# Kernel tuning notes

Measured on AMD Instinct MI355X. Metric: run time of the kernel, lower is better.

Reference implementation:

```python
import jax, jax.numpy as jnp
import numpy as np

D_MODEL = 384
D_STATE = 64
D_CONV = 3
EXPAND = 2
HEADDIM = 64
NGROUPS = 1
CHUNK = 256
D_INNER = EXPAND * D_MODEL            # 768
NHEADS = D_INNER // HEADDIM           # 12
CONV_DIM = D_INNER + 2 * NGROUPS * D_STATE   # 896
D_IN_PROJ = 2 * D_INNER + 2 * NGROUPS * D_STATE + NHEADS  # 1676
EPS = 1e-5


def setup_inputs() -> dict:
    key = jax.random.key(0)
    ks = jax.random.split(key, 8)
    B, H, W = 16, 32, 32
    u = jax.random.normal(ks[0], (B, D_MODEL, H, W), jnp.float32)
    in_proj_w = jax.random.normal(ks[1], (D_IN_PROJ, D_MODEL), jnp.float32) / np.sqrt(D_MODEL)
    conv_w = jax.random.normal(ks[2], (CONV_DIM, 1, D_CONV, D_CONV), jnp.float32) / np.sqrt(D_CONV * D_CONV)
    conv_b = jax.random.normal(ks[3], (CONV_DIM,), jnp.float32) * 0.01
    # dt_bias init as in Mamba2.__init__
    dt = jnp.exp(jax.random.uniform(ks[4], (NHEADS,)) * (np.log(0.1) - np.log(0.001)) + np.log(0.001))
    dt = jnp.clip(dt, 1e-4, None)
    dt_bias = dt + jnp.log(-jnp.expm1(-dt))
    A_log = jnp.log(jax.random.uniform(ks[5], (NHEADS,), minval=1.0, maxval=16.0))
    D = jnp.ones((NHEADS,), jnp.float32)
    norm_w = jnp.ones((D_INNER,), jnp.float32)
    norm_b = jnp.zeros((D_INNER,), jnp.float32)
    out_proj_w = jax.random.normal(ks[6], (D_MODEL, D_INNER), jnp.float32) / np.sqrt(D_INNER)
    return {"u": u, "in_proj_w": in_proj_w, "conv_w": conv_w, "conv_b": conv_b,
            "dt_bias": dt_bias, "A_log": A_log, "D": D, "norm_w": norm_w,
            "norm_b": norm_b, "out_proj_w": out_proj_w}


def _chunk_scan(x, dt, A, Bm, Cm):
    """SSD chunked scan. x:(b,l,h,p) dt:(b,l,h) A:(h,) Bm,Cm:(b,l,g,n) -> (b,l,h,p)"""
    b, l, h, p = x.shape
    nc = l // CHUNK
    xc = x.reshape(b, nc, CHUNK, h, p)
    dtc = dt.reshape(b, nc, CHUNK, h)
    hpg = h // NGROUPS
    Bh = jnp.repeat(Bm.reshape(b, nc, CHUNK, NGROUPS, D_STATE), hpg, axis=3)  # (b,c,cs,h,n)
    Ch = jnp.repeat(Cm.reshape(b, nc, CHUNK, NGROUPS, D_STATE), hpg, axis=3)
    dA = dtc * A                                  # (b,c,cs,h)
    dA_cs = jnp.cumsum(dA, axis=2)                # cumulative log-decay within chunk
    # ---- intra-chunk (masked, attention-like) ----
    Lmat = jnp.exp(dA_cs[:, :, :, None, :] - dA_cs[:, :, None, :, :])  # (b,c,i,j,h)
    causal = jnp.tril(jnp.ones((CHUNK, CHUNK), bool))
    att = jnp.einsum('bcihn,bcjhn->bcijh', Ch, Bh) * Lmat * dtc[:, :, None, :, :]
    att = jnp.where(causal[None, None, :, :, None], att, 0.0)
    y_intra = jnp.einsum('bcijh,bcjhp->bcihp', att, xc)
    # ---- per-chunk end states ----
    decay_to_end = jnp.exp(dA_cs[:, :, -1:, :] - dA_cs)                 # (b,c,cs,h)
    states = jnp.einsum('bcjhn,bcjh,bcjhp->bchpn', Bh, decay_to_end * dtc, xc)
    chunk_decay = jnp.exp(dA_cs[:, :, -1, :])                           # (b,c,h)
    # ---- inter-chunk recurrence over the (few) chunks ----
    def step(carry, inp):
        st, dec = inp
        new = carry * dec[:, :, None, None] + st
        return new, carry  # emit state *before* this chunk
    init = jnp.zeros((b, h, p, D_STATE), x.dtype)
    _, prevs = jax.lax.scan(step, init, (jnp.moveaxis(states, 1, 0), jnp.moveaxis(chunk_decay, 1, 0)))
    prev_states = jnp.moveaxis(prevs, 0, 1)                             # (b,c,h,p,n)
    y_inter = jnp.einsum('bcihn,bcih,bchpn->bcihp', Ch, jnp.exp(dA_cs), prev_states)
    return (y_intra + y_inter).reshape(b, l, h, p)


def reference(u, in_proj_w, conv_w, conv_b, dt_bias, A_log, D, norm_w, norm_b, out_proj_w):
    B, C, H, W = u.shape
    L = H * W
    useq = u.reshape(B, C, L).transpose(0, 2, 1)                        # (B,L,C)
    zxbcdt = useq @ in_proj_w.T                                         # (B,L,D_IN_PROJ)
    z = zxbcdt[..., :D_INNER]
    xBC = zxbcdt[..., D_INNER:D_INNER + CONV_DIM]
    dt = jax.nn.softplus(zxbcdt[..., D_INNER + CONV_DIM:] + dt_bias)    # (B,L,NHEADS)
    # depthwise 3x3 conv over (H,W)
    xBC = xBC.reshape(B, H, W, CONV_DIM)
    kern = jnp.transpose(conv_w, (2, 3, 1, 0))                          # HWIO, groups=CONV_DIM
    xBC = jax.lax.conv_general_dilated(xBC, kern, (1, 1), 'SAME',
                                       dimension_numbers=('NHWC', 'HWIO', 'NHWC'),
                                       feature_group_count=CONV_DIM) + conv_b
    xBC = jax.nn.silu(xBC).reshape(B, L, CONV_DIM)
    x = xBC[..., :D_INNER].reshape(B, L, NHEADS, HEADDIM)
    Bm = xBC[..., D_INNER:D_INNER + NGROUPS * D_STATE].reshape(B, L, NGROUPS, D_STATE)
    Cm = xBC[..., D_INNER + NGROUPS * D_STATE:].reshape(B, L, NGROUPS, D_STATE)
    A = -jnp.exp(A_log)
    y = _chunk_scan(x, dt, A, Bm, Cm) + D[None, None, :, None] * x      # D skip per head
    y = y.reshape(B, L, D_INNER)
    # LayerNorm then gate by z (no activation on z, matching source)
    mu = jnp.mean(y, axis=-1, keepdims=True)
    var = jnp.var(y, axis=-1, keepdims=True)
    y = (y - mu) / jnp.sqrt(var + EPS) * norm_w + norm_b
    y = y * z
    out = y @ out_proj_w.T                                              # (B,L,C)
    return out.reshape(B, H, W, C).transpose(0, 3, 1, 2)
```

## Files before the change

### kernel.cpp

```cpp
#include <hip/hip_runtime.h>
#include <hip/hip_bf16.h>

#define B_    16
#define L_    1024
#define DM    384
#define DIP   1676
#define NIP   1664
#define DI    768
#define CONVD 896
#define NH    12
#define HD    64
#define DS    64
#define NCH   4
#define CH    256
#define EPS_  1e-5f

typedef unsigned short u16;
typedef unsigned int   u32;
typedef __attribute__((ext_vector_type(8))) _Float16 f16x8;
typedef __attribute__((ext_vector_type(4))) float f32x4;

union U4 { uint4 v; u16 s[8]; };

#define SWZ(row, slot) (((row) << 7) + ((((slot) ^ ((row) & 7)) & 7) << 4))

__device__ __forceinline__ u16 f2h(float v) { return __builtin_bit_cast(u16, (_Float16)v); }
__device__ __forceinline__ float h2f(u16 h) { return (float)__builtin_bit_cast(_Float16, h); }
__device__ __forceinline__ void hsplit(float v, u16& h, u16& l) {
  _Float16 hh = (_Float16)v;
  _Float16 ll = (_Float16)(v - (float)hh);
  h = __builtin_bit_cast(u16, hh);
  l = __builtin_bit_cast(u16, ll);
}

__global__ __launch_bounds__(256) void k_cvtA(const float* __restrict__ u,
                                              u16* __restrict__ Ah)
{
  __shared__ float Ls[32][129];
  const int t  = threadIdx.x;
  const int l0 = blockIdx.x * 128;
  const int k0 = blockIdx.y * 32;
  const int b  = blockIdx.z;
#pragma unroll
  for (int r = 0; r < 4; ++r) {
    int idx = r * 256 + t;
    int kk = idx >> 5, q = idx & 31;
    float4 v = *(const float4*)&u[((size_t)(b * DM + k0 + kk)) * L_ + l0 + q * 4];
    Ls[kk][q * 4 + 0] = v.x; Ls[kk][q * 4 + 1] = v.y;
    Ls[kk][q * 4 + 2] = v.z; Ls[kk][q * 4 + 3] = v.w;
  }
  __syncthreads();
#pragma unroll
  for (int it = 0; it < 2; ++it) {
    int task = it * 256 + t;
    int l = task >> 2, kq = (task & 3) * 8;
    u32 hw[4];
#pragma unroll
    for (int j = 0; j < 4; ++j) {
      u16 h0 = f2h(Ls[kq + 2 * j + 0][l]);
      u16 h1 = f2h(Ls[kq + 2 * j + 1][l]);
      hw[j] = (u32)h0 | ((u32)h1 << 16);
    }
    size_t off = ((size_t)(b * L_ + l0 + l)) * DM + k0 + kq;
    *(uint4*)&Ah[off] = make_uint4(hw[0], hw[1], hw[2], hw[3]);
  }
}

__global__ __launch_bounds__(256) void k_cvtWh(const float* __restrict__ W,
                                               u16* __restrict__ Wh, int total4)
{
  int i = blockIdx.x * 256 + threadIdx.x;
  if (i >= total4) return;
  int e = i * 4;
  float4 v = *(const float4*)&W[e];
  u16 h[4] = {f2h(v.x), f2h(v.y), f2h(v.z), f2h(v.w)};
  *(uint2*)&Wh[e] = make_uint2((u32)h[0] | ((u32)h[1] << 16), (u32)h[2] | ((u32)h[3] << 16));
}

__global__ __launch_bounds__(256) void k_dtp(
    const float* __restrict__ u, const float* __restrict__ ipw,
    const float* __restrict__ dtb, const float* __restrict__ A_log,
    float* __restrict__ dt, float* __restrict__ dAcs, float* __restrict__ cdecay)
{
  __shared__ float wdt[DM];
  __shared__ float ws4[4];
  const int bc = blockIdx.x;
  const int h  = blockIdx.y;
  const int b  = bc >> 2, l0 = (bc & 3) * 256;
  const int t  = threadIdx.x;
  const int lane = t & 63, w = t >> 6;
  for (int i = t; i < DM; i += 256) wdt[i] = ipw[(size_t)(NIP + h) * DM + i];
  __syncthreads();
  const float* ub = u + (size_t)b * DM * L_ + l0 + t;
  float acc = 0.f;
#pragma unroll 8
  for (int k = 0; k < DM; ++k)
    acc = fmaf(ub[(size_t)k * L_], wdt[k], acc);
  const size_t row = (size_t)bc * 256 + t;
  float logit = acc + dtb[h];
  float dtv = (logit > 20.f) ? logit : log1pf(expf(logit));
  dt[row * NH + h] = dtv;
  float xv = dtv * (-expf(A_log[h]));
#pragma unroll
  for (int off = 1; off < 64; off <<= 1) {
    float y = __shfl_up(xv, off, 64);
    if (lane >= off) xv += y;
  }
  if (lane == 63) ws4[w] = xv;
  __syncthreads();
  float add = 0.f;
#pragma unroll
  for (int i = 0; i < 4; ++i) if (i < w) add += ws4[i];
  xv += add;
  dAcs[row * NH + h] = xv;
  if (t == 255) cdecay[bc * NH + h] = expf(xv);
}

#define STAGE2(bufbase, k0) do {                                                                \
  _Pragma("unroll")                                                                             \
  for (int i_ = 0; i_ < 2; ++i_) {                                                              \
    int S_ = i_ * 256 + t;                                                                      \
    int m_ = S_ >> 2;                                                                           \
    int g_ = (S_ ^ (m_ >> 1)) & 3;                                                              \
    size_t goff_ = (size_t)m_ * DM + (k0) + g_ * 8;                                             \
    __builtin_amdgcn_global_load_lds((const __attribute__((address_space(1))) u32*)(g0 + goff_),\
        (__attribute__((address_space(3))) u32*)(lds + (bufbase) + S_ * 8), 16, 0, 0);          \
    __builtin_amdgcn_global_load_lds((const __attribute__((address_space(1))) u32*)(g2 + goff_),\
        (__attribute__((address_space(3))) u32*)(lds + (bufbase) + 4096 + S_ * 8), 16, 0, 0);   \
  }                                                                                             \
} while (0)

__global__ __launch_bounds__(256) void k_gemm1(
    const u16* __restrict__ Ah,
    const u16* __restrict__ Wh,
    u16* __restrict__ z, u16* __restrict__ xBC)
{
  __shared__ u16 lds[16384];
  const int t = threadIdx.x;
  const int lane = t & 63, wid = t >> 6;
  const int wr = wid >> 1, wc = wid & 1;
  const int gg = lane >> 4, mlo = lane & 15;
  const int m0 = blockIdx.x * 128, n0 = blockIdx.y * 128;
  f32x4 acc[4][4];
#pragma unroll
  for (int i = 0; i < 4; ++i)
#pragma unroll
    for (int j = 0; j < 4; ++j) acc[i][j] = (f32x4){0.f, 0.f, 0.f, 0.f};
  const u16* g0 = Ah + (size_t)m0 * DM;
  const u16* g2 = Wh + (size_t)n0 * DM;
  STAGE2(0, 0);
  __syncthreads();
  int cur = 0;
  for (int kt = 0; kt < DM / 32; ++kt) {
    if (kt + 1 < DM / 32) STAGE2((cur ^ 1) * 8192, (kt + 1) * 32);
    const char* ldsb = (const char*)lds + cur * 16384;
    f16x8 fa[4], fb[4];
#pragma unroll
    for (int mf = 0; mf < 4; ++mf) {
      int m = wr * 64 + mf * 16 + mlo;
      int off = m * 64 + (((gg ^ (m >> 1)) & 3) << 4);
      fa[mf]  = *(const f16x8*)(ldsb + off);
    }
#pragma unroll
    for (int nf = 0; nf < 4; ++nf) {
      int n = wc * 64 + nf * 16 + mlo;
      int off = n * 64 + (((gg ^ (n >> 1)) & 3) << 4);
      fb[nf]  = *(const f16x8*)(ldsb + 8192 + off);
    }
#pragma unroll
    for (int mf = 0; mf < 4; ++mf)
#pragma unroll
      for (int nf = 0; nf < 4; ++nf)
        acc[mf][nf] = __builtin_amdgcn_mfma_f32_16x16x32_f16(fa[mf], fb[nf], acc[mf][nf], 0, 0, 0);
    __syncthreads();
    cur ^= 1;
  }
  const int rb = m0 + wr * 64 + (lane >> 4) * 4;
  const int cb = n0 + wc * 64 + mlo;
#pragma unroll
  for (int mf = 0; mf < 4; ++mf)
#pragma unroll
    for (int nf = 0; nf < 4; ++nf) {
      int col = cb + nf * 16;
#pragma unroll
      for (int r = 0; r < 4; ++r) {
        int row = rb + mf * 16 + r;
        float v = acc[mf][nf][r];
        if (col < DI) z[(size_t)row * DI + col] = f2h(v);
        else xBC[(size_t)row * CONVD + (col - DI)] = f2h(v);
      }
    }
}

#define STAGE3B(bufbase, k0) do {                                                               \
  _Pragma("unroll")                                                                             \
  for (int i_ = 0; i_ < 2; ++i_) {                                                              \
    int S_ = i_ * 256 + t;                                                                      \
    int m_ = S_ >> 2;                                                                           \
    int g_ = (S_ ^ (m_ >> 1)) & 3;                                                              \
    size_t goff_ = (size_t)m_ * DI + (k0) + g_ * 8;                                             \
    __builtin_amdgcn_global_load_lds((const __attribute__((address_space(1))) u32*)(g0 + goff_),\
        (__attribute__((address_space(3))) u32*)(lds + (bufbase) + S_ * 8), 16, 0, 0);          \
    __builtin_amdgcn_global_load_lds((const __attribute__((address_space(1))) u32*)(g1 + goff_),\
        (__attribute__((address_space(3))) u32*)(lds + (bufbase) + 4096 + S_ * 8), 16, 0, 0);   \
    __builtin_amdgcn_global_load_lds((const __attribute__((address_space(1))) u32*)(g2 + goff_),\
        (__attribute__((address_space(3))) u32*)(lds + (bufbase) + 8192 + S_ * 8), 16, 0, 0);   \
  }                                                                                             \
} while (0)

__global__ __launch_bounds__(256) void k_gemm2(
    const u16* __restrict__ Ah, const u16* __restrict__ Al,
    const u16* __restrict__ Bh,
    float* __restrict__ out)
{
  __shared__ u16 lds[24576];
  const int t = threadIdx.x;
  const int lane = t & 63, wid = t >> 6;
  const int wr = wid >> 1, wc = wid & 1;
  const int gg = lane >> 4, mlo = lane & 15;
  const int m0 = blockIdx.x * 128, n0 = blockIdx.y * 128;
  f32x4 acc[4][4];
#pragma unroll
  for (int i = 0; i < 4; ++i)
#pragma unroll
    for (int j = 0; j < 4; ++j) acc[i][j] = (f32x4){0.f, 0.f, 0.f, 0.f};
  const u16* g0 = Ah + (size_t)m0 * DI;
  const u16* g1 = Al + (size_t)m0 * DI;
  const u16* g2 = Bh + (size_t)n0 * DI;
  STAGE3B(0, 0);
  __syncthreads();
  int cur = 0;
  for (int kt = 0; kt < DI / 32; ++kt) {
    if (kt + 1 < DI / 32) STAGE3B((cur ^ 1) * 12288, (kt + 1) * 32);
    const char* ldsb = (const char*)lds + cur * 24576;
    f16x8 fa[4], fal[4], fb[4];
#pragma unroll
    for (int mf = 0; mf < 4; ++mf) {
      int m = wr * 64 + mf * 16 + mlo;
      int off = m * 64 + (((gg ^ (m >> 1)) & 3) << 4);
      fa[mf]  = *(const f16x8*)(ldsb + off);
      fal[mf] = *(const f16x8*)(ldsb + 8192 + off);
    }
#pragma unroll
    for (int nf = 0; nf < 4; ++nf) {
      int n = wc * 64 + nf * 16 + mlo;
      int off = n * 64 + (((gg ^ (n >> 1)) & 3) << 4);
      fb[nf]  = *(const f16x8*)(ldsb + 16384 + off);
    }
#pragma unroll
    for (int mf = 0; mf < 4; ++mf)
#pragma unroll
      for (int nf = 0; nf < 4; ++nf) {
        acc[mf][nf] = __builtin_amdgcn_mfma_f32_16x16x32_f16(fa[mf],  fb[nf], acc[mf][nf], 0, 0, 0);
        acc[mf][nf] = __builtin_amdgcn_mfma_f32_16x16x32_f16(fal[mf], fb[nf], acc[mf][nf], 0, 0, 0);
      }
    __syncthreads();
    cur ^= 1;
  }
  const int rb = m0 + wr * 64 + (lane >> 4) * 4;
  const int cb = n0 + wc * 64 + mlo;
#pragma unroll
  for (int mf = 0; mf < 4; ++mf)
#pragma unroll
    for (int nf = 0; nf < 4; ++nf) {
      int col = cb + nf * 16;
#pragma unroll
      for (int r = 0; r < 4; ++r) {
        int row = rb + mf * 16 + r;
        int b = row >> 10, l = row & 1023;
        out[((size_t)(b * DM + col)) * L_ + l] = acc[mf][nf][r];
      }
    }
}

#define CC 16
__global__ __launch_bounds__(256) void k_conv(
    const u16* __restrict__ xBC, const float* __restrict__ cw,
    const float* __restrict__ cb,
    u16* __restrict__ XTh,
    u16* __restrict__ Bh,
    u16* __restrict__ Chh)
{
  __shared__ float Ls[18][32][CC];
  const int t  = threadIdx.x;
  const int c0 = blockIdx.x * CC;
  const int h0 = blockIdx.y * 16;
  const int b  = blockIdx.z;
#pragma unroll
  for (int k = 0; k < 9; ++k) {
    int f = k * 256 + t;
    int fc4 = f & 3, fw = (f >> 2) & 31, fr = f >> 7;
    int h = h0 + fr - 1;
    U4 v; v.v = make_uint4(0, 0, 0, 0);
    if (h >= 0 && h < 32) {
      uint2 p = *(const uint2*)&xBC[((size_t)(b * 1024 + h * 32 + fw)) * CONVD + c0 + fc4 * 4];
      v.v.x = p.x; v.v.y = p.y;
    }
    Ls[fr][fw][fc4 * 4 + 0] = h2f(v.s[0]);
    Ls[fr][fw][fc4 * 4 + 1] = h2f(v.s[1]);
    Ls[fr][fw][fc4 * 4 + 2] = h2f(v.s[2]);
    Ls[fr][fw][fc4 * 4 + 3] = h2f(v.s[3]);
  }
  const int c4 = t & 3;
  const int w  = (t >> 2) & 31;
  const int hb = t >> 7;
  float wt[4][9];
  float bias[4];
#pragma unroll
  for (int j = 0; j < 4; ++j) {
    int c = c0 + c4 * 4 + j;
    bias[j] = cb[c];
#pragma unroll
    for (int kb = 0; kb < 9; ++kb) wt[j][kb] = cw[c * 9 + kb];
  }
  __syncthreads();
  const bool isx = (c0 < DI);
  u16 xh16[8][4];
#pragma unroll
  for (int k = 0; k < 8; ++k) {
    int h = hb * 8 + k;
    float acc[4] = {bias[0], bias[1], bias[2], bias[3]};
#pragma unroll
    for (int dh = 0; dh < 3; ++dh) {
#pragma unroll
      for (int dw = -1; dw <= 1; ++dw) {
        int ww = w + dw;
        if (ww < 0 || ww > 31) continue;
        const float* p = &Ls[h + dh][ww][c4 * 4];
        int kb = dh * 3 + (dw + 1);
#pragma unroll
        for (int j = 0; j < 4; ++j) acc[j] = fmaf(p[j], wt[j][kb], acc[j]);
      }
    }
    float s4[4];
#pragma unroll
    for (int j = 0; j < 4; ++j) { float v = acc[j]; s4[j] = v / (1.f + expf(-v)); }
    if (isx) {
#pragma unroll
      for (int j = 0; j < 4; ++j) xh16[k][j] = f2h(s4[j]);
    } else {
      size_t row = (size_t)b * 1024 + (h0 + h) * 32 + w;
      u16 hv[4] = {f2h(s4[0]), f2h(s4[1]), f2h(s4[2]), f2h(s4[3])};
      uint2 hp = make_uint2((u32)hv[0] | ((u32)hv[1] << 16), (u32)hv[2] | ((u32)hv[3] << 16));
      int c = c0 + c4 * 4;
      if (c < DI + DS) *(uint2*)&Bh[row * DS + (c - DI)] = hp;
      else             *(uint2*)&Chh[row * DS + (c - DI - DS)] = hp;
    }
  }
  if (isx) {
    __syncthreads();
    u16* Ls2 = (u16*)Ls;
#pragma unroll
    for (int k = 0; k < 8; ++k) {
      int pos = (hb * 8 + k) * 32 + w;
#pragma unroll
      for (int j = 0; j < 4; ++j)
        Ls2[(c4 * 4 + j) * 512 + pos] = xh16[k][j];
    }
    __syncthreads();
    const int hh = c0 >> 6;
    const int pb = c0 & 63;
#pragma unroll
    for (int i = 0; i < 4; ++i) {
      int cid = i * 256 + t;
      int pl = cid >> 6, rem = cid & 63;
      int jbl = rem >> 3, slot = rem & 7;
      int labs = h0 * 32 + jbl * 64;
      size_t tile = ((size_t)(b * 4 + (labs >> 8)) * NH + hh) * 4 + ((labs >> 6) & 3);
      *(uint4*)((char*)XTh + tile * 8192 + SWZ(pb + pl, slot)) =
          *(const uint4*)&Ls2[pl * 512 + jbl * 64 + slot * 8];
    }
  }
}

#define STAGE_XT(tileByte) do {                                                                   \
  _Pragma("unroll")                                                                               \
  for (int i_ = 0; i_ < 2; ++i_) {                                                                \
    int S_ = i_ * 256 + t;                                                                        \
    __builtin_amdgcn_global_load_lds(                                                             \
        (const __attribute__((address_space(1))) u32*)((const char*)XTh + (tileByte) + S_ * 16),  \
        (__attribute__((address_space(3))) u32*)((char*)Xh_t + S_ * 16), 16, 0, 0);               \
  }                                                                                               \
} while (0)

__global__ __launch_bounds__(256) void k_states(
    const u16* __restrict__ XTh,
    const u16* __restrict__ Bh,
    const float* __restrict__ dt, const float* __restrict__ dAcs,
    float* __restrict__ states)
{
  __shared__ u16 bpackB[64 * 65];
  __shared__ u16 BTh_t[4096];
  __shared__ u16 Xh_t[4096];
  __shared__ float wall[256];
  const int bc = blockIdx.x;
  const int hh = blockIdx.y;
  const int t  = threadIdx.x;
  const int lane = t & 63, w = t >> 6;
  const int mlo = lane & 15, gg = lane >> 4;
  const int r = t >> 2, q = (t & 3) * 16;
  const size_t base = (size_t)bc * 256;
  const float last = dAcs[(base + 255) * NH + hh];
  wall[t] = __expf(last - dAcs[(base + t) * NH + hh]) * dt[(base + t) * NH + hh];
  f32x4 acc[4];
#pragma unroll
  for (int i = 0; i < 4; ++i) acc[i] = (f32x4){0.f, 0.f, 0.f, 0.f};
  for (int jt = 0; jt < 4; ++jt) {
    const int j0 = jt * 64;
    __syncthreads();
    STAGE_XT(((size_t)(bc * NH + hh) * 4 + jt) * 8192);
    {
      const u16* bhp = &Bh[(size_t)(base + j0 + r) * DS + q];
      U4 H0, H1;
      H0.v = *(const uint4*)bhp; H1.v = *(const uint4*)(bhp + 8);
#pragma unroll
      for (int k = 0; k < 8; ++k) {
        bpackB[r * 65 + q + k]     = H0.s[k];
        bpackB[r * 65 + q + 8 + k] = H1.s[k];
      }
    }
    __syncthreads();
#pragma unroll
    for (int c = 0; c < 2; ++c) {
      U4 BH;
#pragma unroll
      for (int jj = 0; jj < 8; ++jj) {
        int j = q + c * 8 + jj;
        BH.s[jj] = f2h(h2f(bpackB[j * 65 + r]) * wall[j0 + j]);
      }
      *(uint4*)((char*)BTh_t + SWZ(r, (q >> 3) + c)) = BH.v;
    }
    __syncthreads();
#pragma unroll
    for (int s = 0; s < 2; ++s) {
      f16x8 fah = *(const f16x8*)((const char*)Xh_t + SWZ(w * 16 + mlo, s * 4 + gg));
#pragma unroll
      for (int nf = 0; nf < 4; ++nf) {
        f16x8 fbh = *(const f16x8*)((const char*)BTh_t + SWZ(nf * 16 + mlo, s * 4 + gg));
        acc[nf] = __builtin_amdgcn_mfma_f32_16x16x32_f16(fah, fbh, acc[nf], 0, 0, 0);
      }
    }
  }
  const size_t sb = ((size_t)(bc * NH + hh)) << 12;
#pragma unroll
  for (int nf = 0; nf < 4; ++nf)
#pragma unroll
    for (int reg = 0; reg < 4; ++reg) {
      int p = w * 16 + (lane >> 4) * 4 + reg;
      int n = nf * 16 + mlo;
      states[sb + (size_t)p * 64 + n] = acc[nf][reg];
    }
}

__global__ __launch_bounds__(256) void k_scanc(
    const float* __restrict__ states, const float* __restrict__ cdecay,
    float* __restrict__ prev)
{
  int tid = blockIdx.x * 256 + threadIdx.x;
  int pn  = tid & 4095;
  int rem = tid >> 12;
  int hh  = rem % NH;
  int b   = rem / NH;
  float carry = 0.f;
#pragma unroll
  for (int c = 0; c < 4; ++c) {
    size_t idx = ((size_t)((b * 4 + c) * NH + hh) << 12) + pn;
    prev[idx] = carry;
    carry = carry * cdecay[(b * 4 + c) * NH + hh] + states[idx];
  }
}

__global__ __launch_bounds__(256) void k_y(
    const u16* __restrict__ XTh,
    const u16* __restrict__ Chg, const u16* __restrict__ Bhg,
    const float* __restrict__ dtp, const float* __restrict__ dAcs,
    const float* __restrict__ prev, const float* __restrict__ Dp,
    u16* __restrict__ y)
{
  __shared__ u16 Pb_t[4096];
  __shared__ u16 Xh_t[4096];
  __shared__ u16 att_t[4096];
  __shared__ float dAc_s[256], dt_s[256], ei_s[128];
  const int bc = blockIdx.x;
  const int hh = blockIdx.y;
  const int z  = blockIdx.z;
  const int it0 = z * 2;
  const int t  = threadIdx.x;
  const int lane = t & 63, w = t >> 6;
  const int mlo = lane & 15, gg = lane >> 4;
  const int r = t >> 2, q = (t & 3) * 16;
  const int slot0 = q >> 3;
  const size_t base = (size_t)bc * 256;
  {
    float da = dAcs[(base + t) * NH + hh];
    dAc_s[t] = da;
    dt_s[t]  = dtp[(base + t) * NH + hh];
    if (t < 128) ei_s[t] = __expf(dAcs[(base + z * 128 + t) * NH + hh]);
  }
  {
    const float* pp = &prev[(((size_t)(bc * NH + hh)) << 12) + (size_t)r * 64 + q];
    U4 H0, H1;
#pragma unroll
    for (int k = 0; k < 16; ++k) {
      u16 h = f2h(pp[k]);
      if (k < 8) H0.s[k] = h; else H1.s[k - 8] = h;
    }
    *(uint4*)((char*)Pb_t + SWZ(r, slot0))     = H0.v;
    *(uint4*)((char*)Pb_t + SWZ(r, slot0 + 1)) = H1.v;
  }
  __syncthreads();
  f16x8 fc[2][2];
#pragma unroll
  for (int iti = 0; iti < 2; ++iti)
#pragma unroll
    for (int s = 0; s < 2; ++s)
      fc[iti][s] = *(const f16x8*)&Chg[(size_t)(base + (it0 + iti) * 64 + w * 16 + mlo) * DS +
                                       (s * 4 + gg) * 8];
  f32x4 accy[2][4];
#pragma unroll
  for (int i = 0; i < 2; ++i)
#pragma unroll
    for (int j = 0; j < 4; ++j) accy[i][j] = (f32x4){0.f, 0.f, 0.f, 0.f};
#pragma unroll
  for (int s = 0; s < 2; ++s)
#pragma unroll
    for (int pf = 0; pf < 4; ++pf) {
      f16x8 fph = *(const f16x8*)((const char*)Pb_t + SWZ(pf * 16 + mlo, s * 4 + gg));
#pragma unroll
      for (int iti = 0; iti < 2; ++iti)
        accy[iti][pf] = __builtin_amdgcn_mfma_f32_16x16x32_f16(fc[iti][s], fph, accy[iti][pf], 0, 0, 0);
    }
  const int ilb = w * 16 + (lane >> 4) * 4;
#pragma unroll
  for (int iti = 0; iti < 2; ++iti)
#pragma unroll
    for (int pf = 0; pf < 4; ++pf)
#pragma unroll
      for (int reg = 0; reg < 4; ++reg)
        accy[iti][pf][reg] *= ei_s[iti * 64 + ilb + reg];

  u32 xdv[2][8];
  for (int jt = 0; jt <= it0 + 1; ++jt) {
    __syncthreads();
    STAGE_XT(((size_t)(bc * NH + hh) * 4 + jt) * 8192);
    {
      const u16* bh = &Bhg[(size_t)(base + jt * 64 + r) * DS + q];
      U4 V0, V1;
      V0.v = *(const uint4*)bh; V1.v = *(const uint4*)(bh + 8);
      float wj = dt_s[jt * 64 + r];
#pragma unroll
      for (int k = 0; k < 8; ++k) {
        V0.s[k] = f2h(h2f(V0.s[k]) * wj);
        V1.s[k] = f2h(h2f(V1.s[k]) * wj);
      }
      *(uint4*)((char*)Pb_t + SWZ(r, slot0))     = V0.v;
      *(uint4*)((char*)Pb_t + SWZ(r, slot0 + 1)) = V1.v;
    }
    __syncthreads();
#pragma unroll
    for (int iti = 0; iti < 2; ++iti) {
      if (jt == it0 + iti) {
#pragma unroll
        for (int pf = 0; pf < 4; ++pf)
#pragma unroll
          for (int rp = 0; rp < 2; ++rp) {
            int j0l = ilb + rp * 2;
            u16 a = *(const u16*)((const char*)Xh_t + SWZ(pf * 16 + mlo, j0l >> 3) + (j0l & 7) * 2);
            u16 b2 = *(const u16*)((const char*)Xh_t + SWZ(pf * 16 + mlo, (j0l + 1) >> 3) + ((j0l + 1) & 7) * 2);
            xdv[iti][pf * 2 + rp] = (u32)a | ((u32)b2 << 16);
          }
      }
    }
#pragma unroll
    for (int iti = 0; iti < 2; ++iti) {
      const int ita = it0 + iti;
      if (jt > ita) continue;
      f32x4 g[4];
#pragma unroll
      for (int i = 0; i < 4; ++i) g[i] = (f32x4){0.f, 0.f, 0.f, 0.f};
#pragma unroll
      for (int s = 0; s < 2; ++s)
#pragma unroll
        for (int jf = 0; jf < 4; ++jf) {
          f16x8 fbh = *(const f16x8*)((const char*)Pb_t + SWZ(jf * 16 + mlo, s * 4 + gg));
          g[jf] = __builtin_amdgcn_mfma_f32_16x16x32_f16(fc[iti][s], fbh, g[jf], 0, 0, 0);
        }
#pragma unroll
      for (int jf = 0; jf < 4; ++jf)
#pragma unroll
        for (int reg = 0; reg < 4; ++reg) {
          int il = ita * 64 + ilb + reg;
          int jl = jt * 64 + jf * 16 + mlo;
          float av = (jl <= il) ? g[jf][reg] * __expf(dAc_s[il] - dAc_s[jl]) : 0.f;
          *(u16*)((char*)att_t + SWZ(il & 63, (jl & 63) >> 3) + (jl & 7) * 2) = f2h(av);
        }
#pragma unroll
      for (int s = 0; s < 2; ++s) {
        f16x8 fa = *(const f16x8*)((const char*)att_t + SWZ(w * 16 + mlo, s * 4 + gg));
#pragma unroll
        for (int pf = 0; pf < 4; ++pf) {
          f16x8 fxh = *(const f16x8*)((const char*)Xh_t + SWZ(pf * 16 + mlo, s * 4 + gg));
          accy[iti][pf] = __builtin_amdgcn_mfma_f32_16x16x32_f16(fa, fxh, accy[iti][pf], 0, 0, 0);
        }
      }
    }
  }
  const float Dh = Dp[hh];
#pragma unroll
  for (int iti = 0; iti < 2; ++iti)
#pragma unroll
    for (int pf = 0; pf < 4; ++pf)
#pragma unroll
      for (int reg = 0; reg < 4; ++reg) {
        size_t row = base + (it0 + iti) * 64 + ilb + reg;
        int col = hh * HD + pf * 16 + mlo;
        u32 pk = xdv[iti][pf * 2 + (reg >> 1)];
        u16 xv = (reg & 1) ? (u16)(pk >> 16) : (u16)pk;
        y[row * DI + col] = f2h(accy[iti][pf][reg] + Dh * h2f(xv));
      }
}

__global__ __launch_bounds__(256) void k_norm(
    const u16* __restrict__ z, const float* __restrict__ nw,
    const float* __restrict__ nb, const u16* __restrict__ y,
    u16* __restrict__ yh, u16* __restrict__ yl)
{
  __shared__ float rs[4], rq[4];
  const size_t row = blockIdx.x;
  const int t = threadIdx.x;
  float v[3];
  float s = 0.f, sq = 0.f;
#pragma unroll
  for (int r = 0; r < 3; ++r) {
    v[r] = h2f(y[row * DI + r * 256 + t]);
    s += v[r];
    sq = fmaf(v[r], v[r], sq);
  }
#pragma unroll
  for (int off = 32; off > 0; off >>= 1) {
    s  += __shfl_down(s, off, 64);
    sq += __shfl_down(sq, off, 64);
  }
  const int wid = t >> 6, lane = t & 63;
  if (lane == 0) { rs[wid] = s; rq[wid] = sq; }
  __syncthreads();
  if (t == 0) {
    rs[0] = rs[0] + rs[1] + rs[2] + rs[3];
    rq[0] = rq[0] + rq[1] + rq[2] + rq[3];
  }
  __syncthreads();
  const float mu   = rs[0] * (1.f / DI);
  const float var  = rq[0] * (1.f / DI) - mu * mu;
  const float rstd = 1.f / sqrtf(var + EPS_);
#pragma unroll
  for (int r = 0; r < 3; ++r) {
    int d = r * 256 + t;
    float o = (v[r] - mu) * rstd * nw[d] + nb[d];
    float p = o * h2f(z[row * DI + d]);
    u16 h, l;
    hsplit(p, h, l);
    yh[row * DI + d] = h;
    yl[row * DI + d] = l;
  }
}

extern "C" void kernel_launch(void* const* d_in, const int* in_sizes, int n_in,
                              void* d_out, int out_size, void* d_ws, size_t ws_size,
                              hipStream_t stream)
{
  const float* u    = (const float*)d_in[0];
  const float* ipw  = (const float*)d_in[1];
  const float* cw   = (const float*)d_in[2];
  const float* cb   = (const float*)d_in[3];
  const float* dtb  = (const float*)d_in[4];
  const float* Alog = (const float*)d_in[5];
  const float* Dp   = (const float*)d_in[6];
  const float* nw   = (const float*)d_in[7];
  const float* nb   = (const float*)d_in[8];
  const float* opw  = (const float*)d_in[9];
  float* out = (float*)d_out;

  float* ws = (float*)d_ws;
  size_t off = 0;
  u16*   z16     = (u16*)(ws + off); off += (size_t)B_ * L_ * DI / 2;
  u16*   xBC16   = (u16*)(ws + off); off += (size_t)B_ * L_ * CONVD / 2;
  float* dt_buf  = ws + off; off += (size_t)B_ * L_ * NH;
  float* x_buf   = ws + off; off += (size_t)B_ * L_ * DI;
  u16*   y16     = (u16*)(ws + off); off += (size_t)B_ * L_ * DI / 2;
  u16*   Bh_buf  = (u16*)(ws + off); off += (size_t)B_ * L_ * DS / 2;
  u16*   Ch_buf  = (u16*)(ws + off); off += (size_t)B_ * L_ * DS / 2;
  float* dAcs    = ws + off; off += (size_t)B_ * L_ * NH;
  float* cdec    = ws + off; off += (size_t)B_ * NCH * NH;
  float* st_buf  = ws + off; off += (size_t)B_ * NCH * NH * HD * DS;
  float* pv_buf  = ws + off; off += (size_t)B_ * NCH * NH * HD * DS;
  u16*   Woh     = (u16*)(ws + off); off += (size_t)DM * DI / 2;
  u16*   XTh_buf = (u16*)(ws + off); off += (size_t)B_ * NCH * NH * 4 * 4096 / 2;

  u16* Ah = (u16*)x_buf;
  u16* Whip = Ah + (size_t)B_ * L_ * DM;
  u16* yh = (u16*)x_buf;
  u16* yl = yh + (size_t)B_ * L_ * DI;

  hipLaunchKernelGGL(k_cvtA, dim3(8, 12, 16), dim3(256), 0, stream, u, Ah);
  hipLaunchKernelGGL(k_cvtWh, dim3((NIP * DM / 4 + 255) / 256), dim3(256), 0, stream,
                     ipw, Whip, NIP * DM / 4);
  hipLaunchKernelGGL(k_cvtWh, dim3((DM * DI / 4 + 255) / 256), dim3(256), 0, stream,
                     opw, Woh, DM * DI / 4);
  hipLaunchKernelGGL(k_dtp, dim3(64, 12), dim3(256), 0, stream,
                     u, ipw, dtb, Alog, dt_buf, dAcs, cdec);
  hipLaunchKernelGGL(k_gemm1, dim3(128, 13), dim3(256), 0, stream,
                     Ah, Whip, z16, xBC16);
  hipLaunchKernelGGL(k_conv, dim3(56, 2, 16), dim3(256), 0, stream,
                     xBC16, cw, cb, XTh_buf, Bh_buf, Ch_buf);
  hipLaunchKernelGGL(k_states, dim3(64, 12), dim3(256), 0, stream,
                     XTh_buf, Bh_buf, dt_buf, dAcs, st_buf);
  hipLaunchKernelGGL(k_scanc, dim3(3072), dim3(256), 0, stream, st_buf, cdec, pv_buf);
  hipLaunchKernelGGL(k_y, dim3(64, 12, 2), dim3(256), 0, stream,
                     XTh_buf, Ch_buf, Bh_buf, dt_buf, dAcs, pv_buf, Dp, y16);
  hipLaunchKernelGGL(k_norm, dim3(16384), dim3(256), 0, stream, z16, nw, nb, y16, yh, yl);
  hipLaunchKernelGGL(k_gemm2, dim3(128, 3), dim3(256), 0, stream, yh, yl, Woh, out);
}
```

Measured before the change: 205.1 us.

## Deepen gemm1 LDS pipeline to four buffers and merge k_y z-split blocks

In k_gemm1, the double-buffered K loop becomes a 4-slot ring buffer with two tiles prefetched ahead. Each step waits with a partial vmcnt and one raw barrier instead of two __syncthreads, so more load latency can be hidden at the cost of doubling LDS per block. In k_y, the two z-blocks per (chunk, head) are merged into one block that handles all four 64-row tiles. This removes the duplicated staging of X and B tiles (z=1 previously restaged tiles 0-1) but halves the grid to 768 blocks and doubles the accumulator registers.

```diff
diff --git a/kernel.cpp b/kernel.cpp
--- a/kernel.cpp
+++ b/kernel.cpp
@@ -135,7 +135,7 @@
     const u16* __restrict__ Wh,
     u16* __restrict__ z, u16* __restrict__ xBC)
 {
-  __shared__ u16 lds[16384];
+  __shared__ u16 lds[32768];
   const int t = threadIdx.x;
   const int lane = t & 63, wid = t >> 6;
   const int wr = wid >> 1, wc = wid & 1;
@@ -148,12 +148,15 @@
     for (int j = 0; j < 4; ++j) acc[i][j] = (f32x4){0.f, 0.f, 0.f, 0.f};
   const u16* g0 = Ah + (size_t)m0 * DM;
   const u16* g2 = Wh + (size_t)n0 * DM;
-  STAGE2(0, 0);
-  __syncthreads();
-  int cur = 0;
-  for (int kt = 0; kt < DM / 32; ++kt) {
-    if (kt + 1 < DM / 32) STAGE2((cur ^ 1) * 8192, (kt + 1) * 32);
-    const char* ldsb = (const char*)lds + cur * 16384;
+  const int NT = DM / 32;
+  STAGE2(0 * 8192, 0 * 32);
+  STAGE2(1 * 8192, 1 * 32);
+  for (int kt = 0; kt < NT; ++kt) {
+    int ks = kt + 2; if (ks > NT - 1) ks = NT - 1;
+    STAGE2(((kt + 2) & 3) * 8192, ks * 32);
+    asm volatile("s_waitcnt vmcnt(8)" ::: "memory");
+    __builtin_amdgcn_s_barrier();
+    const char* ldsb = (const char*)lds + (kt & 3) * 16384;
     f16x8 fa[4], fb[4];
 #pragma unroll
     for (int mf = 0; mf < 4; ++mf) {
@@ -172,8 +175,6 @@
 #pragma unroll
       for (int nf = 0; nf < 4; ++nf)
         acc[mf][nf] = __builtin_amdgcn_mfma_f32_16x16x32_f16(fa[mf], fb[nf], acc[mf][nf], 0, 0, 0);
-    __syncthreads();
-    cur ^= 1;
   }
   const int rb = m0 + wr * 64 + (lane >> 4) * 4;
   const int cb = n0 + wc * 64 + mlo;
@@ -480,11 +481,9 @@
   __shared__ u16 Pb_t[4096];
   __shared__ u16 Xh_t[4096];
   __shared__ u16 att_t[4096];
-  __shared__ float dAc_s[256], dt_s[256], ei_s[128];
+  __shared__ float dAc_s[256], dt_s[256], ei_s[256];
   const int bc = blockIdx.x;
   const int hh = blockIdx.y;
-  const int z  = blockIdx.z;
-  const int it0 = z * 2;
   const int t  = threadIdx.x;
   const int lane = t & 63, w = t >> 6;
   const int mlo = lane & 15, gg = lane >> 4;
@@ -495,7 +494,7 @@
     float da = dAcs[(base + t) * NH + hh];
     dAc_s[t] = da;
     dt_s[t]  = dtp[(base + t) * NH + hh];
-    if (t < 128) ei_s[t] = __expf(dAcs[(base + z * 128 + t) * NH + hh]);
+    ei_s[t]  = __expf(da);
   }
   {
     const float* pp = &prev[(((size_t)(bc * NH + hh)) << 12) + (size_t)r * 64 + q];
@@ -509,16 +508,16 @@
     *(uint4*)((char*)Pb_t + SWZ(r, slot0 + 1)) = H1.v;
   }
   __syncthreads();
-  f16x8 fc[2][2];
-#pragma unroll
-  for (int iti = 0; iti < 2; ++iti)
+  f16x8 fc[4][2];
+#pragma unroll
+  for (int iti = 0; iti < 4; ++iti)
 #pragma unroll
     for (int s = 0; s < 2; ++s)
-      fc[iti][s] = *(const f16x8*)&Chg[(size_t)(base + (it0 + iti) * 64 + w * 16 + mlo) * DS +
+      fc[iti][s] = *(const f16x8*)&Chg[(size_t)(base + iti * 64 + w * 16 + mlo) * DS +
                                        (s * 4 + gg) * 8];
-  f32x4 accy[2][4];
-#pragma unroll
-  for (int i = 0; i < 2; ++i)
+  f32x4 accy[4][4];
+#pragma unroll
+  for (int i = 0; i < 4; ++i)
 #pragma unroll
     for (int j = 0; j < 4; ++j) accy[i][j] = (f32x4){0.f, 0.f, 0.f, 0.f};
 #pragma unroll
@@ -527,20 +526,20 @@
     for (int pf = 0; pf < 4; ++pf) {
       f16x8 fph = *(const f16x8*)((const char*)Pb_t + SWZ(pf * 16 + mlo, s * 4 + gg));
 #pragma unroll
-      for (int iti = 0; iti < 2; ++iti)
+      for (int iti = 0; iti < 4; ++iti)
         accy[iti][pf] = __builtin_amdgcn_mfma_f32_16x16x32_f16(fc[iti][s], fph, accy[iti][pf], 0, 0, 0);
     }
   const int ilb = w * 16 + (lane >> 4) * 4;
 #pragma unroll
-  for (int iti = 0; iti < 2; ++iti)
+  for (int iti = 0; iti < 4; ++iti)
 #pragma unroll
     for (int pf = 0; pf < 4; ++pf)
 #pragma unroll
       for (int reg = 0; reg < 4; ++reg)
         accy[iti][pf][reg] *= ei_s[iti * 64 + ilb + reg];
 
-  u32 xdv[2][8];
-  for (int jt = 0; jt <= it0 + 1; ++jt) {
+  u32 xdv[4][8];
+  for (int jt = 0; jt < 4; ++jt) {
     __syncthreads();
     STAGE_XT(((size_t)(bc * NH + hh) * 4 + jt) * 8192);
     {
@@ -558,8 +557,8 @@
     }
     __syncthreads();
 #pragma unroll
-    for (int iti = 0; iti < 2; ++iti) {
-      if (jt == it0 + iti) {
+    for (int iti = 0; iti < 4; ++iti) {
+      if (jt == iti) {
 #pragma unroll
         for (int pf = 0; pf < 4; ++pf)
 #pragma unroll
@@ -572,9 +571,8 @@
       }
     }
 #pragma unroll
-    for (int iti = 0; iti < 2; ++iti) {
-      const int ita = it0 + iti;
-      if (jt > ita) continue;
+    for (int iti = 0; iti < 4; ++iti) {
+      if (jt > iti) continue;
       f32x4 g[4];
 #pragma unroll
       for (int i = 0; i < 4; ++i) g[i] = (f32x4){0.f, 0.f, 0.f, 0.f};
@@ -589,7 +587,7 @@
       for (int jf = 0; jf < 4; ++jf)
 #pragma unroll
         for (int reg = 0; reg < 4; ++reg) {
-          int il = ita * 64 + ilb + reg;
+          int il = iti * 64 + ilb + reg;
           int jl = jt * 64 + jf * 16 + mlo;
           float av = (jl <= il) ? g[jf][reg] * __expf(dAc_s[il] - dAc_s[jl]) : 0.f;
           *(u16*)((char*)att_t + SWZ(il & 63, (jl & 63) >> 3) + (jl & 7) * 2) = f2h(av);
@@ -607,12 +605,12 @@
   }
   const float Dh = Dp[hh];
 #pragma unroll
-  for (int iti = 0; iti < 2; ++iti)
+  for (int iti = 0; iti < 4; ++iti)
 #pragma unroll
     for (int pf = 0; pf < 4; ++pf)
 #pragma unroll
       for (int reg = 0; reg < 4; ++reg) {
-        size_t row = base + (it0 + iti) * 64 + ilb + reg;
+        size_t row = base + iti * 64 + ilb + reg;
         int col = hh * HD + pf * 16 + mlo;
         u32 pk = xdv[iti][pf * 2 + (reg >> 1)];
         u16 xv = (reg & 1) ? (u16)(pk >> 16) : (u16)pk;
@@ -715,7 +713,7 @@
   hipLaunchKernelGGL(k_states, dim3(64, 12), dim3(256), 0, stream,
                      XTh_buf, Bh_buf, dt_buf, dAcs, st_buf);
   hipLaunchKernelGGL(k_scanc, dim3(3072), dim3(256), 0, stream, st_buf, cdec, pv_buf);
-  hipLaunchKernelGGL(k_y, dim3(64, 12, 2), dim3(256), 0, stream,
+  hipLaunchKernelGGL(k_y, dim3(64, 12), dim3(256), 0, stream,
                      XTh_buf, Ch_buf, Bh_buf, dt_buf, dAcs, pv_buf, Dp, y16);
   hipLaunchKernelGGL(k_norm, dim3(16384), dim3(256), 0, stream, z16, nw, nb, y16, yh, yl);
   hipLaunchKernelGGL(k_gemm2, dim3(128, 3), dim3(256), 0, stream, yh, yl, Woh, out);
```

Result: slower. 215.5 us (+5.1%).
